# Kernel tuning notes

Hardware: AMD Instinct MI355X
Metric: run time of the kernel (lower is better)

Reference implementation:

```python
import jax, jax.numpy as jnp
import numpy as np

N = 100000


def _gcn_prep(edge_index, n):
    # add self-loops, compute symmetric normalization (PyG gcn_norm defaults)
    loops = jnp.arange(n, dtype=edge_index.dtype)
    src = jnp.concatenate([edge_index[0], loops])
    dst = jnp.concatenate([edge_index[1], loops])
    deg = jax.ops.segment_sum(jnp.ones_like(src, dtype=jnp.float32), dst, num_segments=n)
    dinv = jnp.where(deg > 0, jax.lax.rsqrt(deg), 0.0)
    norm = dinv[src] * dinv[dst]  # [E + n]
    return src, dst, norm


def _gcn_layer(x, W, b, src, dst, norm, n):
    h = x @ W                              # [n, out]
    msgs = h[src] * norm[:, None]          # gather + scale, [E+n, out]
    agg = jax.ops.segment_sum(msgs, dst, num_segments=n)
    return agg + b


def setup_inputs() -> dict:
    key = jax.random.key(0)
    ks = jax.random.split(key, 8)
    E = 3200000
    x = jax.random.normal(ks[0], (N, 1), dtype=jnp.float32)
    edge_index = jax.random.randint(ks[1], (2, E), 0, N, dtype=jnp.int64)
    W1 = jax.random.normal(ks[2], (1, 16), dtype=jnp.float32) * (1.0 / np.sqrt(1))
    b1 = jax.random.normal(ks[3], (16,), dtype=jnp.float32) * 0.01
    W2 = jax.random.normal(ks[4], (16, 8), dtype=jnp.float32) * (1.0 / np.sqrt(16))
    b2 = jax.random.normal(ks[5], (8,), dtype=jnp.float32) * 0.01
    Wfc = jax.random.normal(ks[6], (8, 1), dtype=jnp.float32) * (1.0 / np.sqrt(8))
    bfc = jax.random.normal(ks[7], (1,), dtype=jnp.float32) * 0.01
    return {"x": x, "edge_index": edge_index, "W1": W1, "b1": b1,
            "W2": W2, "b2": b2, "Wfc": Wfc, "bfc": bfc}


def reference(x, edge_index, W1, b1, W2, b2, Wfc, bfc):
    n = x.shape[0]
    src, dst, norm = _gcn_prep(edge_index, n)
    h = jax.nn.relu(_gcn_layer(x, W1, b1, src, dst, norm, n))   # [N, 16]
    h = jax.nn.relu(_gcn_layer(h, W2, b2, src, dst, norm, n))   # [N, 8]
    out = h[-1] @ Wfc + bfc                                     # fc applied to last node only
    return out
```

## Files before the change

### kernel.cpp

```cpp
#include <hip/hip_runtime.h>


#define S1CAP 2048
#define DCAP  192
#define L2CAP 65536
#define HASHSZ 512
#define GRID 768
#define NSUB 16

__global__ __launch_bounds__(256)
void k_pass1(const int* __restrict__ src, const int* __restrict__ dst,
             int E4, int E, int n, int* __restrict__ cnts,
             int* __restrict__ S1, unsigned* __restrict__ bm1,
             int* __restrict__ Dlist) {
    int gid = blockIdx.x * 256 + threadIdx.x;
    const int stride = GRID * 256;
    const int tgt = n - 1;
    for (int j = gid; j < E4; j += stride) {
        int4 d4 = ((const int4*)dst)[j];
        int dd[4] = {d4.x, d4.y, d4.z, d4.w};
#pragma unroll
        for (int k = 0; k < 4; ++k) {
            if (dd[k] == tgt) {
                int s = src[j * 4 + k];
                int p = atomicAdd(&cnts[0], 1);
                if (p < S1CAP) S1[p] = s;
                unsigned bit = 1u << (s & 31);
                unsigned old = atomicOr(&bm1[s >> 5], bit);
                if (!(old & bit)) {
                    int q = atomicAdd(&cnts[1], 1);
                    if (q < DCAP) Dlist[q] = s;
                }
            }
        }
    }
    if (gid == 0) {
        for (int e = E4 * 4; e < E; ++e) {
            if (dst[e] == tgt) {
                int s = src[e];
                int p = atomicAdd(&cnts[0], 1);
                if (p < S1CAP) S1[p] = s;
                unsigned bit = 1u << (s & 31);
                unsigned old = atomicOr(&bm1[s >> 5], bit);
                if (!(old & bit)) {
                    int q = atomicAdd(&cnts[1], 1);
                    if (q < DCAP) Dlist[q] = s;
                }
            }
        }
        unsigned bit = 1u << (tgt & 31);
        unsigned old = atomicOr(&bm1[tgt >> 5], bit);
        if (!(old & bit)) {
            int q = atomicAdd(&cnts[1], 1);
            if (q < DCAP) Dlist[q] = tgt;
        }
    }
}

__global__ __launch_bounds__(256)
void k_pass2(const int* __restrict__ src, const int* __restrict__ dst,
             int E4, int E, const unsigned* __restrict__ bm1,
             int* __restrict__ cnts, unsigned long long* __restrict__ L2,
             unsigned* __restrict__ bm2, int* __restrict__ deg,
             const int* __restrict__ Dlist) {
    int gid = blockIdx.x * 256 + threadIdx.x;
    const int stride = GRID * 256;
    if (gid < DCAP) {
        int cntD = cnts[1]; if (cntD > DCAP) cntD = DCAP;
        if (gid < cntD) {
            int d = Dlist[gid];
            unsigned bit = 1u << (d & 31);
            unsigned old = atomicOr(&bm2[d >> 5], bit);
            if (!(old & bit)) deg[d] = 0;
        }
    }
    for (int j = gid; j < E4; j += stride) {
        int4 d4 = ((const int4*)dst)[j];
        int dd[4] = {d4.x, d4.y, d4.z, d4.w};
#pragma unroll
        for (int k = 0; k < 4; ++k) {
            int d = dd[k];
            if ((bm1[d >> 5] >> (d & 31)) & 1u) {
                int s = src[j * 4 + k];
                int p = atomicAdd(&cnts[2], 1);
                if (p < L2CAP)
                    L2[p] = ((unsigned long long)(unsigned)d << 32) | (unsigned)s;
                unsigned bit = 1u << (s & 31);
                unsigned old = atomicOr(&bm2[s >> 5], bit);
                if (!(old & bit)) deg[s] = 0;
            }
        }
    }
    if (gid == 0) {
        for (int e = E4 * 4; e < E; ++e) {
            int d = dst[e];
            if ((bm1[d >> 5] >> (d & 31)) & 1u) {
                int s = src[e];
                int p = atomicAdd(&cnts[2], 1);
                if (p < L2CAP)
                    L2[p] = ((unsigned long long)(unsigned)d << 32) | (unsigned)s;
                unsigned bit = 1u << (s & 31);
                unsigned old = atomicOr(&bm2[s >> 5], bit);
                if (!(old & bit)) deg[s] = 0;
            }
        }
    }
}

__global__ __launch_bounds__(256)
void k_pass3f(const float* __restrict__ x, const int* __restrict__ dst,
              int E4, int E, int n,
              const unsigned* __restrict__ bm2, int* __restrict__ deg,
              int* __restrict__ cnts, const int* __restrict__ S1,
              const int* __restrict__ Dlist,
              const unsigned long long* __restrict__ L2,
              const float* __restrict__ W1, const float* __restrict__ b1,
              const float* __restrict__ W2, const float* __restrict__ b2,
              const float* __restrict__ Wfc, const float* __restrict__ bfc,
              float* __restrict__ out) {
    const int tid = threadIdx.x;
    const int tgt = n - 1;

    int gid = blockIdx.x * 256 + tid;
    const int stride = GRID * 256;
    for (int j = gid; j < E4; j += stride) {
        int4 d4 = ((const int4*)dst)[j];
        int dd[4] = {d4.x, d4.y, d4.z, d4.w};
#pragma unroll
        for (int k = 0; k < 4; ++k) {
            int d = dd[k];
            if ((bm2[d >> 5] >> (d & 31)) & 1u) atomicAdd(&deg[d], 1);
        }
    }
    if (gid == 0) {
        for (int e = E4 * 4; e < E; ++e) {
            int d = dst[e];
            if ((bm2[d >> 5] >> (d & 31)) & 1u) atomicAdd(&deg[d], 1);
        }
    }

    __shared__ int sLast;
    asm volatile("s_waitcnt vmcnt(0)" ::: "memory");
    __syncthreads();
    if (tid == 0) {
        int last = 0;
        int sub = blockIdx.x % NSUB;
        int quota = GRID / NSUB;
        int so = atomicAdd(&cnts[16 + sub * 32], 1);
        if (so == quota - 1) {
            int ro = atomicAdd(&cnts[16 + NSUB * 32], 1);
            if (ro == NSUB - 1) last = 1;
        }
        sLast = last;
    }
    __syncthreads();
    if (!sLast) return;

    __shared__ int hKey[HASHSZ];
    __shared__ int hVal[HASHSZ];
    __shared__ int sD[DCAP];
    __shared__ float s1D[DCAP];
    __shared__ float gD[DCAP][8];
    __shared__ float sW1[16], sb1[16], sW2[128], agg[8];

    int cnt1 = cnts[0]; if (cnt1 > S1CAP) cnt1 = S1CAP;
    int cntD = cnts[1]; if (cntD > DCAP) cntD = DCAP;
    int cnt2 = cnts[2]; if (cnt2 > L2CAP) cnt2 = L2CAP;

    for (int j = tid; j < HASHSZ; j += 256) hKey[j] = -1;
    for (int j = tid; j < cntD; j += 256) { sD[j] = Dlist[j]; s1D[j] = 0.f; }
    if (tid < 16) { sW1[tid] = W1[tid]; sb1[tid] = b1[tid]; }
    if (tid < 128) sW2[tid] = W2[tid];
    if (tid < 8) agg[tid] = 0.f;
    __syncthreads();
    for (int j = tid; j < cntD; j += 256) {
        int d = sD[j];
        int h = d & (HASHSZ - 1);
        while (true) {
            int prev = atomicCAS(&hKey[h], -1, d);
            if (prev == -1 || prev == d) { hVal[h] = j; break; }
            h = (h + 1) & (HASHSZ - 1);
        }
    }
    __syncthreads();
    for (int e = tid; e < cnt2; e += 256) {
        unsigned long long v = L2[e];
        int s = (int)(v & 0xffffffffu);
        int d = (int)(v >> 32);
        int ds = atomicOr(&deg[s], 0);
        float msg = x[s] * rsqrtf((float)(ds + 1));
        int h = d & (HASHSZ - 1);
        while (hKey[h] != d) h = (h + 1) & (HASHSZ - 1);
        atomicAdd(&s1D[hVal[h]], msg);
    }
    __syncthreads();
    for (int di = tid; di < cntD; di += 256) {
        int d = sD[di];
        int dd = atomicOr(&deg[d], 0);
        float dv = rsqrtf((float)(dd + 1));
        float t = dv * (s1D[di] + x[d] * dv);
        float g8[8] = {0, 0, 0, 0, 0, 0, 0, 0};
#pragma unroll
        for (int c = 0; c < 16; ++c) {
            float h1 = fmaxf(fmaf(t, sW1[c], sb1[c]), 0.f);
#pragma unroll
            for (int j = 0; j < 8; ++j) g8[j] = fmaf(h1, sW2[c * 8 + j], g8[j]);
        }
#pragma unroll
        for (int j = 0; j < 8; ++j) gD[di][j] = dv * g8[j];
    }
    __syncthreads();
    for (int idx = tid; idx < cnt1 * 8; idx += 256) {
        int p = idx >> 3, j = idx & 7;
        int s = S1[p];
        int h = s & (HASHSZ - 1);
        while (hKey[h] != s) h = (h + 1) & (HASHSZ - 1);
        atomicAdd(&agg[j], gD[hVal[h]][j]);
    }
    __syncthreads();
    if (tid == 0) {
        int h = tgt & (HASHSZ - 1);
        while (hKey[h] != tgt) h = (h + 1) & (HASHSZ - 1);
        int it = hVal[h];
        int dt = atomicOr(&deg[tgt], 0);
        float dv = rsqrtf((float)(dt + 1));
        float o = 0.f;
#pragma unroll
        for (int j = 0; j < 8; ++j)
            o += fmaxf(fmaf(dv, agg[j] + gD[it][j], b2[j]), 0.f) * Wfc[j];
        out[0] = o + bfc[0];
    }
}

extern "C" void kernel_launch(void* const* d_in, const int* in_sizes, int n_in,
                              void* d_out, int out_size, void* d_ws, size_t ws_size,
                              hipStream_t stream) {
    const float* x   = (const float*)d_in[0];
    const int*   ei  = (const int*)d_in[1];
    const float* W1  = (const float*)d_in[2];
    const float* b1  = (const float*)d_in[3];
    const float* W2  = (const float*)d_in[4];
    const float* b2  = (const float*)d_in[5];
    const float* Wfc = (const float*)d_in[6];
    const float* bfc = (const float*)d_in[7];
    float* out = (float*)d_out;

    int n = in_sizes[0];
    int E = in_sizes[1] / 2;
    const int* src = ei;
    const int* dst = ei + E;

    auto align16 = [](size_t v) { return (v + 15) & ~(size_t)15; };
    size_t bmBytes = align16(((size_t)(n + 31) / 32) * 4);
    char* ws = (char*)d_ws;
    size_t off = 0;
    unsigned* bm1   = (unsigned*)(ws + off); off += bmBytes;
    unsigned* bm2   = (unsigned*)(ws + off); off += bmBytes;
    int*      cnts  = (int*)(ws + off);      off += 4096;
    size_t zeroBytes = off;
    int*      deg   = (int*)(ws + off);      off += align16((size_t)n * 4);
    int*      S1    = (int*)(ws + off);      off += S1CAP * 4;
    int*      Dlist = (int*)(ws + off);      off += align16(DCAP * 4);
    unsigned long long* L2 = (unsigned long long*)(ws + off); off += (size_t)L2CAP * 8;

    hipMemsetAsync(d_ws, 0, zeroBytes, stream);

    int E4 = E >> 2;

    k_pass1<<<GRID, 256, 0, stream>>>(src, dst, E4, E, n, cnts, S1, bm1, Dlist);
    k_pass2<<<GRID, 256, 0, stream>>>(src, dst, E4, E, bm1, cnts, L2, bm2, deg, Dlist);
    k_pass3f<<<GRID, 256, 0, stream>>>(x, dst, E4, E, n, bm2, deg, cnts, S1,
                                       Dlist, L2, W1, b1, W2, b2, Wfc, bfc, out);
}
```

Measured before the change: 121.1 us.

## Fuse three edge-scan passes into one persistent kernel with grid barriers

Merges the three launches into a single persistent kernel that separates the phases with hierarchical atomic grid barriers, removing two kernel launch gaps. Each block copies the bitmap into shared memory before scanning, replacing global bitmap lookups with LDS reads. The edge loops are also unrolled two-way to keep more loads in flight. The grid barrier assumes all 768 blocks are co-resident, and the 13 KB of shared memory per block could limit occupancy or deadlock if the grid cannot fit.

Result: no change. 121.8 us (+0.5%).

```diff
diff --git a/kernel.cpp b/kernel.cpp
--- a/kernel.cpp
+++ b/kernel.cpp
@@ -5,31 +5,99 @@
 #define DCAP  192
 #define L2CAP 65536
 #define HASHSZ 512
-#define GRID 768
-#define NSUB 16
+#define GRID  768
+#define NSUB  32
+#define BMW   3328
+#define BANK_INTS (NSUB * 32 + 64)
+
+__device__ __forceinline__ int ald(int* p) {
+    return __hip_atomic_load(p, __ATOMIC_RELAXED, __HIP_MEMORY_SCOPE_AGENT);
+}
+__device__ __forceinline__ unsigned aldu(unsigned* p) {
+    return __hip_atomic_load(p, __ATOMIC_RELAXED, __HIP_MEMORY_SCOPE_AGENT);
+}
+__device__ __forceinline__ unsigned long long ald64(unsigned long long* p) {
+    return __hip_atomic_load(p, __ATOMIC_RELAXED, __HIP_MEMORY_SCOPE_AGENT);
+}
+__device__ __forceinline__ void ast(int* p, int v) {
+    __hip_atomic_store(p, v, __ATOMIC_RELAXED, __HIP_MEMORY_SCOPE_AGENT);
+}
+__device__ __forceinline__ void ast64(unsigned long long* p, unsigned long long v) {
+    __hip_atomic_store(p, v, __ATOMIC_RELAXED, __HIP_MEMORY_SCOPE_AGENT);
+}
+
+__device__ __forceinline__ void gridbar(int* bank) {
+    asm volatile("s_waitcnt vmcnt(0)" ::: "memory");
+    __syncthreads();
+    if (threadIdx.x == 0) {
+        int* root = bank + NSUB * 32;
+        int* flag = bank + NSUB * 32 + 32;
+        if (atomicAdd(&bank[(blockIdx.x & (NSUB - 1)) * 32], 1) == GRID / NSUB - 1)
+            if (atomicAdd(root, 1) == NSUB - 1)
+                ast(flag, 1);
+        while (!ald(flag)) __builtin_amdgcn_s_sleep(2);
+    }
+    __syncthreads();
+}
 
 __global__ __launch_bounds__(256)
-void k_pass1(const int* __restrict__ src, const int* __restrict__ dst,
-             int E4, int E, int n, int* __restrict__ cnts,
-             int* __restrict__ S1, unsigned* __restrict__ bm1,
-             int* __restrict__ Dlist) {
-    int gid = blockIdx.x * 256 + threadIdx.x;
+void k_fused(const float* __restrict__ x, const int* __restrict__ src,
+             const int* __restrict__ dst, int E4, int E, int n,
+             int* __restrict__ cnts, int* __restrict__ S1,
+             unsigned* __restrict__ bm1, unsigned* __restrict__ bm2,
+             int* __restrict__ deg, int* __restrict__ Dlist,
+             unsigned long long* __restrict__ L2,
+             const float* __restrict__ W1, const float* __restrict__ b1,
+             const float* __restrict__ W2, const float* __restrict__ b2,
+             const float* __restrict__ Wfc, const float* __restrict__ bfc,
+             float* __restrict__ out) {
+    __shared__ unsigned sBM[BMW];
+    __shared__ int sLast;
+    const int tid = threadIdx.x;
+    const int gid = blockIdx.x * 256 + tid;
     const int stride = GRID * 256;
     const int tgt = n - 1;
-    for (int j = gid; j < E4; j += stride) {
-        int4 d4 = ((const int4*)dst)[j];
-        int dd[4] = {d4.x, d4.y, d4.z, d4.w};
+    const int bmWords = (n + 31) >> 5;
+    const int4* dst4 = (const int4*)dst;
+    int* bank1 = cnts + 64;
+    int* bank2 = bank1 + BANK_INTS;
+    int* bank3 = bank2 + BANK_INTS;
+
+    for (int j = gid; j < E4; j += 2 * stride) {
+        int4 a = dst4[j];
+        int jb = j + stride;
+        bool hb = jb < E4;
+        int4 b;
+        if (hb) b = dst4[jb];
 #pragma unroll
         for (int k = 0; k < 4; ++k) {
-            if (dd[k] == tgt) {
+            int d = k == 0 ? a.x : k == 1 ? a.y : k == 2 ? a.z : a.w;
+            if (d == tgt) {
                 int s = src[j * 4 + k];
                 int p = atomicAdd(&cnts[0], 1);
-                if (p < S1CAP) S1[p] = s;
+                if (p < S1CAP) ast(&S1[p], s);
                 unsigned bit = 1u << (s & 31);
                 unsigned old = atomicOr(&bm1[s >> 5], bit);
                 if (!(old & bit)) {
                     int q = atomicAdd(&cnts[1], 1);
-                    if (q < DCAP) Dlist[q] = s;
+                    if (q < DCAP) ast(&Dlist[q], s);
+                }
+            }
+        }
+        if (hb) {
+#pragma unroll
+            for (int k = 0; k < 4; ++k) {
+                int d = k == 0 ? b.x : k == 1 ? b.y : k == 2 ? b.z : b.w;
+                if (d == tgt) {
+                    int s = src[jb * 4 + k];
+                    int p = atomicAdd(&cnts[0], 1);
+                    if (p < S1CAP) ast(&S1[p], s);
+                    unsigned bit = 1u << (s & 31);
+                    unsigned old = atomicOr(&bm1[s >> 5], bit);
+                    if (!(old & bit)) {
+                        int q = atomicAdd(&cnts[1], 1);
+                        if (q < DCAP) ast(&Dlist[q], s);
+                    }
                 }
             }
         }
@@ -39,12 +107,12 @@
             if (dst[e] == tgt) {
                 int s = src[e];
                 int p = atomicAdd(&cnts[0], 1);
-                if (p < S1CAP) S1[p] = s;
+                if (p < S1CAP) ast(&S1[p], s);
                 unsigned bit = 1u << (s & 31);
                 unsigned old = atomicOr(&bm1[s >> 5], bit);
                 if (!(old & bit)) {
                     int q = atomicAdd(&cnts[1], 1);
-                    if (q < DCAP) Dlist[q] = s;
+                    if (q < DCAP) ast(&Dlist[q], s);
                 }
             }
         }
@@ -52,105 +120,111 @@
         unsigned old = atomicOr(&bm1[tgt >> 5], bit);
         if (!(old & bit)) {
             int q = atomicAdd(&cnts[1], 1);
-            if (q < DCAP) Dlist[q] = tgt;
-        }
-    }
-}
-
-__global__ __launch_bounds__(256)
-void k_pass2(const int* __restrict__ src, const int* __restrict__ dst,
-             int E4, int E, const unsigned* __restrict__ bm1,
-             int* __restrict__ cnts, unsigned long long* __restrict__ L2,
-             unsigned* __restrict__ bm2, int* __restrict__ deg,
-             const int* __restrict__ Dlist) {
-    int gid = blockIdx.x * 256 + threadIdx.x;
-    const int stride = GRID * 256;
+            if (q < DCAP) ast(&Dlist[q], tgt);
+        }
+    }
+
+    gridbar(bank1);
+
+    for (int w = tid; w < bmWords; w += 256) sBM[w] = aldu(&bm1[w]);
+    __syncthreads();
     if (gid < DCAP) {
-        int cntD = cnts[1]; if (cntD > DCAP) cntD = DCAP;
+        int cntD = ald(&cnts[1]); if (cntD > DCAP) cntD = DCAP;
         if (gid < cntD) {
-            int d = Dlist[gid];
+            int d = ald(&Dlist[gid]);
             unsigned bit = 1u << (d & 31);
             unsigned old = atomicOr(&bm2[d >> 5], bit);
-            if (!(old & bit)) deg[d] = 0;
-        }
-    }
-    for (int j = gid; j < E4; j += stride) {
-        int4 d4 = ((const int4*)dst)[j];
-        int dd[4] = {d4.x, d4.y, d4.z, d4.w};
+            if (!(old & bit)) ast(&deg[d], 0);
+        }
+    }
+    for (int j = gid; j < E4; j += 2 * stride) {
+        int4 a = dst4[j];
+        int jb = j + stride;
+        bool hb = jb < E4;
+        int4 b;
+        if (hb) b = dst4[jb];
 #pragma unroll
         for (int k = 0; k < 4; ++k) {
-            int d = dd[k];
-            if ((bm1[d >> 5] >> (d & 31)) & 1u) {
+            int d = k == 0 ? a.x : k == 1 ? a.y : k == 2 ? a.z : a.w;
+            if ((sBM[d >> 5] >> (d & 31)) & 1u) {
                 int s = src[j * 4 + k];
                 int p = atomicAdd(&cnts[2], 1);
                 if (p < L2CAP)
-                    L2[p] = ((unsigned long long)(unsigned)d << 32) | (unsigned)s;
+                    ast64(&L2[p], ((unsigned long long)(unsigned)d << 32) | (unsigned)s);
                 unsigned bit = 1u << (s & 31);
                 unsigned old = atomicOr(&bm2[s >> 5], bit);
-                if (!(old & bit)) deg[s] = 0;
+                if (!(old & bit)) ast(&deg[s], 0);
+            }
+        }
+        if (hb) {
+#pragma unroll
+            for (int k = 0; k < 4; ++k) {
+                int d = k == 0 ? b.x : k == 1 ? b.y : k == 2 ? b.z : b.w;
+                if ((sBM[d >> 5] >> (d & 31)) & 1u) {
+                    int s = src[jb * 4 + k];
+                    int p = atomicAdd(&cnts[2], 1);
+                    if (p < L2CAP)
+                        ast64(&L2[p], ((unsigned long long)(unsigned)d << 32) | (unsigned)s);
+                    unsigned bit = 1u << (s & 31);
+                    unsigned old = atomicOr(&bm2[s >> 5], bit);
+                    if (!(old & bit)) ast(&deg[s], 0);
+                }
             }
         }
     }
     if (gid == 0) {
         for (int e = E4 * 4; e < E; ++e) {
             int d = dst[e];
-            if ((bm1[d >> 5] >> (d & 31)) & 1u) {
+            if ((sBM[d >> 5] >> (d & 31)) & 1u) {
                 int s = src[e];
                 int p = atomicAdd(&cnts[2], 1);
                 if (p < L2CAP)
-                    L2[p] = ((unsigned long long)(unsigned)d << 32) | (unsigned)s;
+                    ast64(&L2[p], ((unsigned long long)(unsigned)d << 32) | (unsigned)s);
                 unsigned bit = 1u << (s & 31);
                 unsigned old = atomicOr(&bm2[s >> 5], bit);
-                if (!(old & bit)) deg[s] = 0;
-            }
-        }
-    }
-}
-
-__global__ __launch_bounds__(256)
-void k_pass3f(const float* __restrict__ x, const int* __restrict__ dst,
-              int E4, int E, int n,
-              const unsigned* __restrict__ bm2, int* __restrict__ deg,
-              int* __restrict__ cnts, const int* __restrict__ S1,
-              const int* __restrict__ Dlist,
-              const unsigned long long* __restrict__ L2,
-              const float* __restrict__ W1, const float* __restrict__ b1,
-              const float* __restrict__ W2, const float* __restrict__ b2,
-              const float* __restrict__ Wfc, const float* __restrict__ bfc,
-              float* __restrict__ out) {
-    const int tid = threadIdx.x;
-    const int tgt = n - 1;
-
-    int gid = blockIdx.x * 256 + tid;
-    const int stride = GRID * 256;
-    for (int j = gid; j < E4; j += stride) {
-        int4 d4 = ((const int4*)dst)[j];
-        int dd[4] = {d4.x, d4.y, d4.z, d4.w};
+                if (!(old & bit)) ast(&deg[s], 0);
+            }
+        }
+    }
+
+    gridbar(bank2);
+
+    __syncthreads();
+    for (int w = tid; w < bmWords; w += 256) sBM[w] = aldu(&bm2[w]);
+    __syncthreads();
+    for (int j = gid; j < E4; j += 2 * stride) {
+        int4 a = dst4[j];
+        int jb = j + stride;
+        bool hb = jb < E4;
+        int4 b;
+        if (hb) b = dst4[jb];
 #pragma unroll
         for (int k = 0; k < 4; ++k) {
-            int d = dd[k];
-            if ((bm2[d >> 5] >> (d & 31)) & 1u) atomicAdd(&deg[d], 1);
+            int d = k == 0 ? a.x : k == 1 ? a.y : k == 2 ? a.z : a.w;
+            if ((sBM[d >> 5] >> (d & 31)) & 1u) atomicAdd(&deg[d], 1);
+        }
+        if (hb) {
+#pragma unroll
+            for (int k = 0; k < 4; ++k) {
+                int d = k == 0 ? b.x : k == 1 ? b.y : k == 2 ? b.z : b.w;
+                if ((sBM[d >> 5] >> (d & 31)) & 1u) atomicAdd(&deg[d], 1);
+            }
         }
     }
     if (gid == 0) {
         for (int e = E4 * 4; e < E; ++e) {
             int d = dst[e];
-            if ((bm2[d >> 5] >> (d & 31)) & 1u) atomicAdd(&deg[d], 1);
-        }
-    }
-
-    __shared__ int sLast;
+            if ((sBM[d >> 5] >> (d & 31)) & 1u) atomicAdd(&deg[d], 1);
+        }
+    }
+
     asm volatile("s_waitcnt vmcnt(0)" ::: "memory");
     __syncthreads();
     if (tid == 0) {
         int last = 0;
-        int sub = blockIdx.x % NSUB;
-        int quota = GRID / NSUB;
-        int so = atomicAdd(&cnts[16 + sub * 32], 1);
-        if (so == quota - 1) {
-            int ro = atomicAdd(&cnts[16 + NSUB * 32], 1);
-            if (ro == NSUB - 1) last = 1;
-        }
+        int* root = bank3 + NSUB * 32;
+        if (atomicAdd(&bank3[(blockIdx.x & (NSUB - 1)) * 32], 1) == GRID / NSUB - 1)
+            if (atomicAdd(root, 1) == NSUB - 1) last = 1;
         sLast = last;
     }
     __syncthreads();
@@ -163,12 +237,12 @@
     __shared__ float gD[DCAP][8];
     __shared__ float sW1[16], sb1[16], sW2[128], agg[8];
 
-    int cnt1 = cnts[0]; if (cnt1 > S1CAP) cnt1 = S1CAP;
-    int cntD = cnts[1]; if (cntD > DCAP) cntD = DCAP;
-    int cnt2 = cnts[2]; if (cnt2 > L2CAP) cnt2 = L2CAP;
+    int cnt1 = ald(&cnts[0]); if (cnt1 > S1CAP) cnt1 = S1CAP;
+    int cntD = ald(&cnts[1]); if (cntD > DCAP) cntD = DCAP;
+    int cnt2 = ald(&cnts[2]); if (cnt2 > L2CAP) cnt2 = L2CAP;
 
     for (int j = tid; j < HASHSZ; j += 256) hKey[j] = -1;
-    for (int j = tid; j < cntD; j += 256) { sD[j] = Dlist[j]; s1D[j] = 0.f; }
+    for (int j = tid; j < cntD; j += 256) { sD[j] = ald(&Dlist[j]); s1D[j] = 0.f; }
     if (tid < 16) { sW1[tid] = W1[tid]; sb1[tid] = b1[tid]; }
     if (tid < 128) sW2[tid] = W2[tid];
     if (tid < 8) agg[tid] = 0.f;
@@ -184,10 +258,10 @@
     }
     __syncthreads();
     for (int e = tid; e < cnt2; e += 256) {
-        unsigned long long v = L2[e];
+        unsigned long long v = ald64(&L2[e]);
         int s = (int)(v & 0xffffffffu);
         int d = (int)(v >> 32);
-        int ds = atomicOr(&deg[s], 0);
+        int ds = ald(&deg[s]);
         float msg = x[s] * rsqrtf((float)(ds + 1));
         int h = d & (HASHSZ - 1);
         while (hKey[h] != d) h = (h + 1) & (HASHSZ - 1);
@@ -196,7 +270,7 @@
     __syncthreads();
     for (int di = tid; di < cntD; di += 256) {
         int d = sD[di];
-        int dd = atomicOr(&deg[d], 0);
+        int dd = ald(&deg[d]);
         float dv = rsqrtf((float)(dd + 1));
         float t = dv * (s1D[di] + x[d] * dv);
         float g8[8] = {0, 0, 0, 0, 0, 0, 0, 0};
@@ -212,7 +286,7 @@
     __syncthreads();
     for (int idx = tid; idx < cnt1 * 8; idx += 256) {
         int p = idx >> 3, j = idx & 7;
-        int s = S1[p];
+        int s = ald(&S1[p]);
         int h = s & (HASHSZ - 1);
         while (hKey[h] != s) h = (h + 1) & (HASHSZ - 1);
         atomicAdd(&agg[j], gD[hVal[h]][j]);
@@ -222,7 +296,7 @@
         int h = tgt & (HASHSZ - 1);
         while (hKey[h] != tgt) h = (h + 1) & (HASHSZ - 1);
         int it = hVal[h];
-        int dt = atomicOr(&deg[tgt], 0);
+        int dt = ald(&deg[tgt]);
         float dv = rsqrtf((float)(dt + 1));
         float o = 0.f;
 #pragma unroll
@@ -254,21 +328,18 @@
     size_t bmBytes = align16(((size_t)(n + 31) / 32) * 4);
     char* ws = (char*)d_ws;
     size_t off = 0;
-    unsigned* bm1   = (unsigned*)(ws + off); off += bmBytes;
-    unsigned* bm2   = (unsigned*)(ws + off); off += bmBytes;
-    int*      cnts  = (int*)(ws + off);      off += 4096;
+    unsigned* bm1  = (unsigned*)(ws + off); off += bmBytes;
+    unsigned* bm2  = (unsigned*)(ws + off); off += bmBytes;
+    int*      cnts = (int*)(ws + off);      off += align16((64 + 3 * BANK_INTS) * 4);
     size_t zeroBytes = off;
-    int*      deg   = (int*)(ws + off);      off += align16((size_t)n * 4);
-    int*      S1    = (int*)(ws + off);      off += S1CAP * 4;
-    int*      Dlist = (int*)(ws + off);      off += align16(DCAP * 4);
+    int*      deg   = (int*)(ws + off);     off += align16((size_t)n * 4);
+    int*      S1    = (int*)(ws + off);     off += S1CAP * 4;
+    int*      Dlist = (int*)(ws + off);     off += align16(DCAP * 4);
     unsigned long long* L2 = (unsigned long long*)(ws + off); off += (size_t)L2CAP * 8;
 
     hipMemsetAsync(d_ws, 0, zeroBytes, stream);
 
     int E4 = E >> 2;
-
-    k_pass1<<<GRID, 256, 0, stream>>>(src, dst, E4, E, n, cnts, S1, bm1, Dlist);
-    k_pass2<<<GRID, 256, 0, stream>>>(src, dst, E4, E, bm1, cnts, L2, bm2, deg, Dlist);
-    k_pass3f<<<GRID, 256, 0, stream>>>(x, dst, E4, E, n, bm2, deg, cnts, S1,
-                                       Dlist, L2, W1, b1, W2, b2, Wfc, bfc, out);
-}
+    k_fused<<<GRID, 256, 0, stream>>>(x, src, dst, E4, E, n, cnts, S1, bm1, bm2,
+                                      deg, Dlist, L2, W1, b1, W2, b2, Wfc, bfc, out);
+}
```
